# Kernel tuning notes

Measured on AMD Instinct MI355X. Metric: run time of the kernel, lower is better.

## Reference

```python
import jax, jax.numpy as jnp
import numpy as np

B, S, E, H = 4, 2048, 1024, 16
D = E // H  # head dim = 64


def setup_inputs() -> dict:
    key0 = jax.random.key(0)
    ks = jax.random.split(key0, 8)
    key = jax.random.normal(ks[0], (B, S, E), dtype=jnp.float32)
    query = jax.random.normal(ks[1], (B, S, E), dtype=jnp.float32)
    value = jax.random.normal(ks[2], (B, S, E), dtype=jnp.float32)
    # causal mask, broadcastable over heads: [B, 1, S, S]; avoids all-masked rows
    mask = jnp.broadcast_to(jnp.tril(jnp.ones((S, S), dtype=jnp.int32)), (B, 1, S, S))
    sc = 1.0 / np.sqrt(E)
    Wq = jax.random.normal(ks[3], (E, E), dtype=jnp.float32) * sc  # nn.Linear weight [out,in]
    Wk = jax.random.normal(ks[4], (E, E), dtype=jnp.float32) * sc
    Wv = jax.random.normal(ks[5], (E, E), dtype=jnp.float32) * sc
    Wo = jax.random.normal(ks[6], (E, E), dtype=jnp.float32) * sc
    bo = jax.random.normal(ks[7], (E,), dtype=jnp.float32) * 0.01
    return {"key": key, "query": query, "value": value, "mask": mask,
            "Wq": Wq, "Wk": Wk, "Wv": Wv, "Wo": Wo, "bo": bo}


def reference(key, query, value, mask, Wq, Wk, Wv, Wo, bo):
    b, s, _ = key.shape
    sq = query.shape[1]
    # projections (nn.Linear: x @ W^T)
    k = (key @ Wk.T).reshape(b, s, H, D).transpose(0, 2, 1, 3)     # [B,H,S,D]
    q = (query @ Wq.T).reshape(b, sq, H, D).transpose(0, 2, 1, 3)  # [B,H,Sq,D]
    v = (value @ Wv.T).reshape(b, s, H, D).transpose(0, 2, 1, 3)   # [B,H,S,D]
    scores = jnp.einsum('bhqd,bhkd->bhqk', q, k)                   # [B,H,Sq,S]
    # original masks BEFORE scaling (-inf survives the divide)
    scores = jnp.where(mask == 0, -jnp.inf, scores)
    scores = scores / jnp.sqrt(jnp.asarray(D, scores.dtype))
    attn = jax.nn.softmax(scores, axis=-1)
    val = jnp.einsum('bhqk,bhkd->bhqd', attn, v)                   # [B,H,Sq,D]
    val = val.transpose(0, 2, 1, 3).reshape(b, s, H * D)           # [B,S,E]
    return val @ Wo.T + bo
```

## Files before the change

### kernel.cpp

```cpp
#include <hip/hip_runtime.h>
#include <hip/hip_bf16.h>
#include <stdint.h>

#define Bk 4
#define Sk 2048
#define Ek 1024
#define Hk 16
#define Dk 64
#define Mk (Bk*Sk)
#define KVB 64

typedef __hip_bfloat16 bf16;
typedef __attribute__((ext_vector_type(8))) short bf16x8;
typedef __attribute__((ext_vector_type(4))) float f32x4;

__device__ __forceinline__ unsigned short f2bf(float f) {
    __hip_bfloat16 h = __float2bfloat16(f);
    return __builtin_bit_cast(unsigned short, h);
}
__device__ __forceinline__ unsigned pack2bf(float a, float b) {
    return (unsigned)f2bf(a) | ((unsigned)f2bf(b) << 16);
}

__device__ __forceinline__ void gld_lds16(const void* g, void* l) {
    __builtin_amdgcn_global_load_lds(
        (const __attribute__((address_space(1))) unsigned int*)g,
        (__attribute__((address_space(3))) unsigned int*)l, 16, 0, 0);
}

__global__ __launch_bounds__(256)
void conv_qkv(const float* __restrict__ q, const float* __restrict__ k,
              const float* __restrict__ v,
              ushort4* __restrict__ qb, ushort4* __restrict__ kb2,
              ushort4* __restrict__ vb)
{
    const int NQ = (Mk * Ek) / 4;
    int i = blockIdx.x * 256 + threadIdx.x;
    const int tot = 3 * NQ;
    for (; i < tot; i += gridDim.x * 256) {
        const float4* sp; ushort4* dp; int j;
        if (i < NQ)            { sp = (const float4*)q; dp = qb;  j = i; }
        else if (i < 2 * NQ)   { sp = (const float4*)k; dp = kb2; j = i - NQ; }
        else                   { sp = (const float4*)v; dp = vb;  j = i - 2 * NQ; }
        float4 x = sp[j];
        ushort4 o; o.x = f2bf(x.x); o.y = f2bf(x.y); o.z = f2bf(x.z); o.w = f2bf(x.w);
        dp[j] = o;
    }
}

__global__ __launch_bounds__(256)
void conv_w(const float* __restrict__ wq, const float* __restrict__ wk,
            const float* __restrict__ wv, const float* __restrict__ wo,
            ushort4* __restrict__ wqb, ushort4* __restrict__ wkb,
            ushort4* __restrict__ wvb, ushort4* __restrict__ wob)
{
    const int NW = (Ek * Ek) / 4;
    int i = blockIdx.x * 256 + threadIdx.x;
    const int tot = 4 * NW;
    for (; i < tot; i += gridDim.x * 256) {
        int rgn = i / NW, j = i - rgn * NW;
        const float4* sp = rgn == 0 ? (const float4*)wq :
                           rgn == 1 ? (const float4*)wk :
                           rgn == 2 ? (const float4*)wv : (const float4*)wo;
        ushort4* dp = rgn == 0 ? wqb : rgn == 1 ? wkb : rgn == 2 ? wvb : wob;
        float sc = (rgn == 0) ? 0.125f * 1.44269504088896f : 1.0f;
        float4 x = sp[j];
        ushort4 o; o.x = f2bf(x.x * sc); o.y = f2bf(x.y * sc);
        o.z = f2bf(x.z * sc); o.w = f2bf(x.w * sc);
        dp[j] = o;
    }
}

template<int EPI>
__global__ __launch_bounds__(256)
void gemm_bt(const bf16* __restrict__ A, const bf16* __restrict__ Bw,
             void* __restrict__ Cout, const float* __restrict__ bias)
{
    __shared__ bf16 As[128 * 64];
    __shared__ bf16 Bs[128 * 64];
    const int t = threadIdx.x, w = t >> 6, lane = t & 63;
    const int lo = lane & 15, hi = lane >> 4;
    const int wm = w >> 1, wn = w & 1;
    const int n0 = blockIdx.x * 128, m0 = blockIdx.y * 128;

    f32x4 acc[4][4] = {};

    const bf16* Ab = A  + (size_t)m0 * Ek;
    const bf16* Bb = Bw + (size_t)n0 * Ek;

    for (int kt = 0; kt < Ek; kt += 64) {
#pragma unroll
        for (int i = 0; i < 4; ++i) {
            int c = (w * 4 + i) * 64 + lane;
            int r = c >> 3, cb = c & 7, scb = cb ^ (r & 7);
            gld_lds16(Ab + (size_t)r * Ek + kt + scb * 8, &As[(w * 4 + i) * 512]);
            gld_lds16(Bb + (size_t)r * Ek + kt + scb * 8, &Bs[(w * 4 + i) * 512]);
        }
        __syncthreads();
#pragma unroll
        for (int kd = 0; kd < 2; ++kd) {
            bf16x8 av[4], bv[4];
#pragma unroll
            for (int mf = 0; mf < 4; ++mf) {
                int r = wm * 64 + mf * 16 + lo;
                int cb = (kd * 4 + hi) ^ (r & 7);
                av[mf] = *(const bf16x8*)&As[r * 64 + cb * 8];
            }
#pragma unroll
            for (int nf = 0; nf < 4; ++nf) {
                int r = wn * 64 + nf * 16 + lo;
                int cb = (kd * 4 + hi) ^ (r & 7);
                bv[nf] = *(const bf16x8*)&Bs[r * 64 + cb * 8];
            }
#pragma unroll
            for (int mf = 0; mf < 4; ++mf)
#pragma unroll
                for (int nf = 0; nf < 4; ++nf)
                    acc[mf][nf] = __builtin_amdgcn_mfma_f32_16x16x32_bf16(
                        av[mf], bv[nf], acc[mf][nf], 0, 0, 0);
        }
        __syncthreads();
    }
#pragma unroll
    for (int mf = 0; mf < 4; ++mf)
#pragma unroll
        for (int nf = 0; nf < 4; ++nf)
#pragma unroll
            for (int r = 0; r < 4; ++r) {
                int m = m0 + wm * 64 + mf * 16 + hi * 4 + r;
                int n = n0 + wn * 64 + nf * 16 + lo;
                float vv = acc[mf][nf][r];
                if constexpr (EPI == 0) {
                    ((bf16*)Cout)[(size_t)m * Ek + n] = __float2bfloat16(vv);
                } else if constexpr (EPI == 1) {
                    int b = m >> 11, s = m & (Sk - 1);
                    ((bf16*)Cout)[((size_t)(b * 1024 + n)) * Sk + s] = __float2bfloat16(vv);
                } else {
                    ((float*)Cout)[(size_t)m * Ek + n] = vv + bias[n];
                }
            }
}

__global__ __launch_bounds__(64)
void attn_fwd1(const bf16* __restrict__ Qp, const bf16* __restrict__ Kp,
               const bf16* __restrict__ Vt, bf16* __restrict__ AO)
{
    __shared__ bf16 Pl[32 * 64];
    const int lane = threadIdx.x;
    const int lo = lane & 15, hi = lane >> 4;
    const int flat = blockIdx.x;
    const int xcd  = flat & 7;
    const int idx  = flat >> 3;
    const int bh   = xcd * 8 + (idx >> 6);
    const int qt   = 63 - (idx & 63);
    const int b = bh >> 4, h = bh & 15;
    const int q0 = qt * 32;
    const int ntiles = q0 / KVB + 1;

    const bf16* Qg = Qp + (size_t)(b * Sk) * Ek + h * 64;
    const bf16* Kg = Kp + (size_t)(b * Sk) * Ek + h * 64;
    const bf16* Vg = Vt + (size_t)(b * 1024 + h * 64) * Sk;

    bf16x8 qf[2][2];
#pragma unroll
    for (int mf = 0; mf < 2; ++mf)
#pragma unroll
        for (int sl = 0; sl < 2; ++sl)
            qf[mf][sl] = *(const bf16x8*)&Qg[(size_t)(q0 + mf * 16 + lo) * Ek + sl * 32 + hi * 8];

    f32x4 acc[2][4] = {};
    float mrow[2] = { -1e30f, -1e30f };
    float lrow[2] = { 0.f, 0.f };

    for (int kt = 0; kt < ntiles; ++kt) {
        const int kb = kt * KVB;
        bf16x8 kfr[4][2], vfr[4][2];
#pragma unroll
        for (int i = 0; i < 4; ++i) {
            const bf16* kr = &Kg[(size_t)(kb + i * 16 + lo) * Ek + hi * 8];
            kfr[i][0] = *(const bf16x8*)kr;
            kfr[i][1] = *(const bf16x8*)(kr + 32);
            const bf16* vr = &Vg[(size_t)(i * 16 + lo) * Sk + kb + hi * 8];
            vfr[i][0] = *(const bf16x8*)vr;
            vfr[i][1] = *(const bf16x8*)(vr + 32);
        }
        f32x4 sT[4][2] = {};
        __builtin_amdgcn_s_setprio(1);
#pragma unroll
        for (int kf = 0; kf < 4; ++kf)
#pragma unroll
            for (int mf = 0; mf < 2; ++mf) {
                sT[kf][mf] = __builtin_amdgcn_mfma_f32_16x16x32_bf16(kfr[kf][0], qf[mf][0], sT[kf][mf], 0, 0, 0);
                sT[kf][mf] = __builtin_amdgcn_mfma_f32_16x16x32_bf16(kfr[kf][1], qf[mf][1], sT[kf][mf], 0, 0, 0);
            }
        __builtin_amdgcn_s_setprio(0);
        if (kb + KVB > q0) {
#pragma unroll
            for (int kf = 0; kf < 4; ++kf)
#pragma unroll
                for (int mf = 0; mf < 2; ++mf)
#pragma unroll
                    for (int r = 0; r < 4; ++r)
                        if (kb + kf * 16 + hi * 4 + r > q0 + mf * 16 + lo)
                            sT[kf][mf][r] = -1e30f;
        }
        float pmax[2];
#pragma unroll
        for (int mf = 0; mf < 2; ++mf) {
            float v0 = fmaxf(fmaxf(sT[0][mf][0], sT[0][mf][1]), fmaxf(sT[0][mf][2], sT[0][mf][3]));
            float v1 = fmaxf(fmaxf(sT[1][mf][0], sT[1][mf][1]), fmaxf(sT[1][mf][2], sT[1][mf][3]));
            float v2 = fmaxf(fmaxf(sT[2][mf][0], sT[2][mf][1]), fmaxf(sT[2][mf][2], sT[2][mf][3]));
            float v3 = fmaxf(fmaxf(sT[3][mf][0], sT[3][mf][1]), fmaxf(sT[3][mf][2], sT[3][mf][3]));
            float v = fmaxf(fmaxf(v0, v1), fmaxf(v2, v3));
            v = fmaxf(v, __shfl_xor(v, 16));
            v = fmaxf(v, __shfl_xor(v, 32));
            pmax[mf] = v;
        }
        bool need = (pmax[0] > mrow[0] + 8.f) || (pmax[1] > mrow[1] + 8.f);
        if (__any(need)) {
            float sf[2];
#pragma unroll
            for (int mf = 0; mf < 2; ++mf) {
                float mn = fmaxf(mrow[mf], pmax[mf]);
                sf[mf] = exp2f(mrow[mf] - mn);
                mrow[mf] = mn;
                lrow[mf] *= sf[mf];
            }
#pragma unroll
            for (int r = 0; r < 4; ++r) {
                float a0 = __shfl(sf[0], hi * 4 + r);
                float a1 = __shfl(sf[1], hi * 4 + r);
#pragma unroll
                for (int nd = 0; nd < 4; ++nd) { acc[0][nd][r] *= a0; acc[1][nd][r] *= a1; }
            }
        }
        float rs[2] = { 0.f, 0.f };
#pragma unroll
        for (int kf = 0; kf < 4; ++kf)
#pragma unroll
            for (int mf = 0; mf < 2; ++mf)
#pragma unroll
                for (int r = 0; r < 4; ++r) {
                    float p = exp2f(sT[kf][mf][r] - mrow[mf]);
                    sT[kf][mf][r] = p;
                    rs[mf] += p;
                }
#pragma unroll
        for (int mf = 0; mf < 2; ++mf) {
            float v = rs[mf];
            v += __shfl_xor(v, 16);
            v += __shfl_xor(v, 32);
            lrow[mf] += v;
        }
#pragma unroll
        for (int mf = 0; mf < 2; ++mf)
#pragma unroll
            for (int kf = 0; kf < 4; ++kf) {
                int q = mf * 16 + lo;
                int chunk = kf * 2 + (hi >> 1);
                int idx2 = q * 64 + ((chunk ^ (q & 7)) * 8) + 4 * (hi & 1);
                uint2 u;
                u.x = pack2bf(sT[kf][mf][0], sT[kf][mf][1]);
                u.y = pack2bf(sT[kf][mf][2], sT[kf][mf][3]);
                *(uint2*)&Pl[idx2] = u;
            }
        bf16x8 pa[2][2];
#pragma unroll
        for (int mf = 0; mf < 2; ++mf)
#pragma unroll
            for (int ks = 0; ks < 2; ++ks) {
                int q = mf * 16 + lo;
                pa[mf][ks] = *(const bf16x8*)&Pl[q * 64 + (((ks * 4 + hi) ^ (q & 7)) * 8)];
            }
        __builtin_amdgcn_s_setprio(1);
#pragma unroll
        for (int mf = 0; mf < 2; ++mf)
#pragma unroll
            for (int nd = 0; nd < 4; ++nd) {
                acc[mf][nd] = __builtin_amdgcn_mfma_f32_16x16x32_bf16(pa[mf][0], vfr[nd][0], acc[mf][nd], 0, 0, 0);
                acc[mf][nd] = __builtin_amdgcn_mfma_f32_16x16x32_bf16(pa[mf][1], vfr[nd][1], acc[mf][nd], 0, 0, 0);
            }
        __builtin_amdgcn_s_setprio(0);
    }
#pragma unroll
    for (int mf = 0; mf < 2; ++mf)
#pragma unroll
        for (int r = 0; r < 4; ++r) {
            float il = 1.0f / __shfl(lrow[mf], hi * 4 + r);
            int q = q0 + mf * 16 + hi * 4 + r;
#pragma unroll
            for (int nd = 0; nd < 4; ++nd)
                AO[(size_t)(b * Sk + q) * Ek + h * 64 + nd * 16 + lo] =
                    __float2bfloat16(acc[mf][nd][r] * il);
        }
}

extern "C" void kernel_launch(void* const* d_in, const int* in_sizes, int n_in,
                              void* d_out, int out_size, void* d_ws, size_t ws_size,
                              hipStream_t stream)
{
    (void)in_sizes; (void)n_in; (void)out_size; (void)ws_size;
    const float* key   = (const float*)d_in[0];
    const float* query = (const float*)d_in[1];
    const float* value = (const float*)d_in[2];
    const float* Wq = (const float*)d_in[4];
    const float* Wk = (const float*)d_in[5];
    const float* Wv = (const float*)d_in[6];
    const float* Wo = (const float*)d_in[7];
    const float* bo = (const float*)d_in[8];

    char* ws = (char*)d_ws;
    bf16* Vin = (bf16*)ws; ws += (size_t)Mk * Ek * 2;
    bf16* Wqb = (bf16*)ws; ws += (size_t)Ek * Ek * 2;
    bf16* Wkb = (bf16*)ws; ws += (size_t)Ek * Ek * 2;
    bf16* Wvb = (bf16*)ws; ws += (size_t)Ek * Ek * 2;
    bf16* Wob = (bf16*)ws; ws += (size_t)Ek * Ek * 2;
    bf16* Qp  = (bf16*)ws; ws += (size_t)Mk * Ek * 2;
    bf16* Kp  = (bf16*)ws; ws += (size_t)Mk * Ek * 2;
    bf16* Vt  = (bf16*)ws; ws += (size_t)Mk * Ek * 2;
    bf16* AO  = (bf16*)ws; ws += (size_t)Mk * Ek * 2;

    bf16* Qin = (bf16*)d_out;
    bf16* Kin = Qin + (size_t)Mk * Ek;

    conv_qkv<<<4096, 256, 0, stream>>>(query, key, value,
                                       (ushort4*)Qin, (ushort4*)Kin, (ushort4*)Vin);
    conv_w<<<2048, 256, 0, stream>>>(Wq, Wk, Wv, Wo,
                                     (ushort4*)Wqb, (ushort4*)Wkb, (ushort4*)Wvb, (ushort4*)Wob);

    dim3 gg(Ek / 128, Mk / 128);
    gemm_bt<0><<<gg, 256, 0, stream>>>(Qin, Wqb, Qp, nullptr);
    gemm_bt<0><<<gg, 256, 0, stream>>>(Kin, Wkb, Kp, nullptr);
    gemm_bt<1><<<gg, 256, 0, stream>>>(Vin, Wvb, Vt, nullptr);

    attn_fwd1<<<dim3(Sk / 32 * Hk * Bk), 64, 0, stream>>>(Qp, Kp, Vt, AO);

    gemm_bt<2><<<gg, 256, 0, stream>>>(AO, Wob, d_out, bo);
}
```

Baseline: 438.3 us.

## Share K/V tiles across four waves via double-buffered LDS in attention

Replaces the single-wave attention kernel, which loaded K and V straight from global memory into registers, with a 256-thread block of four waves covering 128 queries. The waves share swizzled K/V tiles staged in LDS with global_load_lds and double buffering. This cuts redundant global K/V traffic fourfold and overlaps the next tile's load with compute. The cost is a block-wide barrier every tile and idle waves on causal diagonal tiles. Blocks are also fewer and larger, which may reduce load balance.

```diff
diff --git a/kernel.cpp b/kernel.cpp
--- a/kernel.cpp
+++ b/kernel.cpp
@@ -9,6 +9,7 @@
 #define Dk 64
 #define Mk (Bk*Sk)
 #define KVB 64
+#define QCH 128
 
 typedef __hip_bfloat16 bf16;
 typedef __attribute__((ext_vector_type(8))) short bf16x8;
@@ -141,21 +142,25 @@
             }
 }
 
-__global__ __launch_bounds__(64)
-void attn_fwd1(const bf16* __restrict__ Qp, const bf16* __restrict__ Kp,
-               const bf16* __restrict__ Vt, bf16* __restrict__ AO)
-{
-    __shared__ bf16 Pl[32 * 64];
-    const int lane = threadIdx.x;
+__global__ __launch_bounds__(256)
+void attn_fwd4x(const bf16* __restrict__ Qp, const bf16* __restrict__ Kp,
+                const bf16* __restrict__ Vt, bf16* __restrict__ AO)
+{
+    __shared__ bf16 Kl[2][KVB * 64];
+    __shared__ bf16 Vl[2][64 * KVB];
+    __shared__ bf16 Pl[4][32 * 64];
+    const int t = threadIdx.x, w = t >> 6, lane = t & 63;
     const int lo = lane & 15, hi = lane >> 4;
     const int flat = blockIdx.x;
     const int xcd  = flat & 7;
     const int idx  = flat >> 3;
-    const int bh   = xcd * 8 + (idx >> 6);
-    const int qt   = 63 - (idx & 63);
+    const int bh   = xcd * 8 + (idx >> 4);
+    const int qc   = 15 - (idx & 15);
     const int b = bh >> 4, h = bh & 15;
-    const int q0 = qt * 32;
-    const int ntiles = q0 / KVB + 1;
+    const int qbase = qc * QCH;
+    const int q0 = qbase + w * 32;
+    const int qe = q0 + 32;
+    const int ntiles = (qbase + QCH) / KVB;
 
     const bf16* Qg = Qp + (size_t)(b * Sk) * Ek + h * 64;
     const bf16* Kg = Kp + (size_t)(b * Sk) * Ek + h * 64;
@@ -172,115 +177,138 @@
     float mrow[2] = { -1e30f, -1e30f };
     float lrow[2] = { 0.f, 0.f };
 
+#pragma unroll
+    for (int i = 0; i < 2; ++i) {
+        int c = w * 128 + i * 64 + lane;
+        int r = c >> 3, cb = c & 7, scb = cb ^ (r & 7);
+        gld_lds16(Kg + (size_t)r * Ek + scb * 8, &Kl[0][(w * 128 + i * 64) * 8]);
+        gld_lds16(Vg + (size_t)r * Sk + scb * 8, &Vl[0][(w * 128 + i * 64) * 8]);
+    }
+    __syncthreads();
+
     for (int kt = 0; kt < ntiles; ++kt) {
         const int kb = kt * KVB;
-        bf16x8 kfr[4][2], vfr[4][2];
-#pragma unroll
-        for (int i = 0; i < 4; ++i) {
-            const bf16* kr = &Kg[(size_t)(kb + i * 16 + lo) * Ek + hi * 8];
-            kfr[i][0] = *(const bf16x8*)kr;
-            kfr[i][1] = *(const bf16x8*)(kr + 32);
-            const bf16* vr = &Vg[(size_t)(i * 16 + lo) * Sk + kb + hi * 8];
-            vfr[i][0] = *(const bf16x8*)vr;
-            vfr[i][1] = *(const bf16x8*)(vr + 32);
-        }
-        f32x4 sT[4][2] = {};
-        __builtin_amdgcn_s_setprio(1);
-#pragma unroll
-        for (int kf = 0; kf < 4; ++kf)
+        const int cur = kt & 1;
+        if (kt + 1 < ntiles) {
+            const int kb2 = kb + KVB;
+#pragma unroll
+            for (int i = 0; i < 2; ++i) {
+                int c = w * 128 + i * 64 + lane;
+                int r = c >> 3, cb = c & 7, scb = cb ^ (r & 7);
+                gld_lds16(Kg + (size_t)(kb2 + r) * Ek + scb * 8,
+                          &Kl[cur ^ 1][(w * 128 + i * 64) * 8]);
+                gld_lds16(Vg + (size_t)r * Sk + kb2 + scb * 8,
+                          &Vl[cur ^ 1][(w * 128 + i * 64) * 8]);
+            }
+        }
+        if (kb < qe) {
+            f32x4 sT[4][2] = {};
+            __builtin_amdgcn_s_setprio(1);
+#pragma unroll
+            for (int kf = 0; kf < 4; ++kf) {
+                int rk = kf * 16 + lo;
+                bf16x8 k0 = *(const bf16x8*)&Kl[cur][rk * 64 + ((0 + hi) ^ (rk & 7)) * 8];
+                bf16x8 k1 = *(const bf16x8*)&Kl[cur][rk * 64 + ((4 + hi) ^ (rk & 7)) * 8];
+#pragma unroll
+                for (int mf = 0; mf < 2; ++mf) {
+                    sT[kf][mf] = __builtin_amdgcn_mfma_f32_16x16x32_bf16(k0, qf[mf][0], sT[kf][mf], 0, 0, 0);
+                    sT[kf][mf] = __builtin_amdgcn_mfma_f32_16x16x32_bf16(k1, qf[mf][1], sT[kf][mf], 0, 0, 0);
+                }
+            }
+            __builtin_amdgcn_s_setprio(0);
+            if (kb + KVB > q0) {
+#pragma unroll
+                for (int kf = 0; kf < 4; ++kf)
+#pragma unroll
+                    for (int mf = 0; mf < 2; ++mf)
+#pragma unroll
+                        for (int r = 0; r < 4; ++r)
+                            if (kb + kf * 16 + hi * 4 + r > q0 + mf * 16 + lo)
+                                sT[kf][mf][r] = -1e30f;
+            }
+            float pmax[2];
 #pragma unroll
             for (int mf = 0; mf < 2; ++mf) {
-                sT[kf][mf] = __builtin_amdgcn_mfma_f32_16x16x32_bf16(kfr[kf][0], qf[mf][0], sT[kf][mf], 0, 0, 0);
-                sT[kf][mf] = __builtin_amdgcn_mfma_f32_16x16x32_bf16(kfr[kf][1], qf[mf][1], sT[kf][mf], 0, 0, 0);
-            }
-        __builtin_amdgcn_s_setprio(0);
-        if (kb + KVB > q0) {
+                float v0 = fmaxf(fmaxf(sT[0][mf][0], sT[0][mf][1]), fmaxf(sT[0][mf][2], sT[0][mf][3]));
+                float v1 = fmaxf(fmaxf(sT[1][mf][0], sT[1][mf][1]), fmaxf(sT[1][mf][2], sT[1][mf][3]));
+                float v2 = fmaxf(fmaxf(sT[2][mf][0], sT[2][mf][1]), fmaxf(sT[2][mf][2], sT[2][mf][3]));
+                float v3 = fmaxf(fmaxf(sT[3][mf][0], sT[3][mf][1]), fmaxf(sT[3][mf][2], sT[3][mf][3]));
+                float v = fmaxf(fmaxf(v0, v1), fmaxf(v2, v3));
+                v = fmaxf(v, __shfl_xor(v, 16));
+                v = fmaxf(v, __shfl_xor(v, 32));
+                pmax[mf] = v;
+            }
+            bool need = (pmax[0] > mrow[0] + 8.f) || (pmax[1] > mrow[1] + 8.f);
+            if (__any(need)) {
+                float sf[2];
+#pragma unroll
+                for (int mf = 0; mf < 2; ++mf) {
+                    float mn = fmaxf(mrow[mf], pmax[mf]);
+                    sf[mf] = exp2f(mrow[mf] - mn);
+                    mrow[mf] = mn;
+                    lrow[mf] *= sf[mf];
+                }
+#pragma unroll
+                for (int r = 0; r < 4; ++r) {
+                    float a0 = __shfl(sf[0], hi * 4 + r);
+                    float a1 = __shfl(sf[1], hi * 4 + r);
+#pragma unroll
+                    for (int nd = 0; nd < 4; ++nd) { acc[0][nd][r] *= a0; acc[1][nd][r] *= a1; }
+                }
+            }
+            float rs[2] = { 0.f, 0.f };
 #pragma unroll
             for (int kf = 0; kf < 4; ++kf)
 #pragma unroll
                 for (int mf = 0; mf < 2; ++mf)
 #pragma unroll
-                    for (int r = 0; r < 4; ++r)
-                        if (kb + kf * 16 + hi * 4 + r > q0 + mf * 16 + lo)
-                            sT[kf][mf][r] = -1e30f;
-        }
-        float pmax[2];
-#pragma unroll
-        for (int mf = 0; mf < 2; ++mf) {
-            float v0 = fmaxf(fmaxf(sT[0][mf][0], sT[0][mf][1]), fmaxf(sT[0][mf][2], sT[0][mf][3]));
-            float v1 = fmaxf(fmaxf(sT[1][mf][0], sT[1][mf][1]), fmaxf(sT[1][mf][2], sT[1][mf][3]));
-            float v2 = fmaxf(fmaxf(sT[2][mf][0], sT[2][mf][1]), fmaxf(sT[2][mf][2], sT[2][mf][3]));
-            float v3 = fmaxf(fmaxf(sT[3][mf][0], sT[3][mf][1]), fmaxf(sT[3][mf][2], sT[3][mf][3]));
-            float v = fmaxf(fmaxf(v0, v1), fmaxf(v2, v3));
-            v = fmaxf(v, __shfl_xor(v, 16));
-            v = fmaxf(v, __shfl_xor(v, 32));
-            pmax[mf] = v;
-        }
-        bool need = (pmax[0] > mrow[0] + 8.f) || (pmax[1] > mrow[1] + 8.f);
-        if (__any(need)) {
-            float sf[2];
+                    for (int r = 0; r < 4; ++r) {
+                        float p = exp2f(sT[kf][mf][r] - mrow[mf]);
+                        sT[kf][mf][r] = p;
+                        rs[mf] += p;
+                    }
 #pragma unroll
             for (int mf = 0; mf < 2; ++mf) {
-                float mn = fmaxf(mrow[mf], pmax[mf]);
-                sf[mf] = exp2f(mrow[mf] - mn);
-                mrow[mf] = mn;
-                lrow[mf] *= sf[mf];
-            }
-#pragma unroll
-            for (int r = 0; r < 4; ++r) {
-                float a0 = __shfl(sf[0], hi * 4 + r);
-                float a1 = __shfl(sf[1], hi * 4 + r);
-#pragma unroll
-                for (int nd = 0; nd < 4; ++nd) { acc[0][nd][r] *= a0; acc[1][nd][r] *= a1; }
-            }
-        }
-        float rs[2] = { 0.f, 0.f };
-#pragma unroll
-        for (int kf = 0; kf < 4; ++kf)
+                float v = rs[mf];
+                v += __shfl_xor(v, 16);
+                v += __shfl_xor(v, 32);
+                lrow[mf] += v;
+            }
 #pragma unroll
             for (int mf = 0; mf < 2; ++mf)
 #pragma unroll
-                for (int r = 0; r < 4; ++r) {
-                    float p = exp2f(sT[kf][mf][r] - mrow[mf]);
-                    sT[kf][mf][r] = p;
-                    rs[mf] += p;
-                }
-#pragma unroll
-        for (int mf = 0; mf < 2; ++mf) {
-            float v = rs[mf];
-            v += __shfl_xor(v, 16);
-            v += __shfl_xor(v, 32);
-            lrow[mf] += v;
-        }
-#pragma unroll
-        for (int mf = 0; mf < 2; ++mf)
-#pragma unroll
-            for (int kf = 0; kf < 4; ++kf) {
-                int q = mf * 16 + lo;
-                int chunk = kf * 2 + (hi >> 1);
-                int idx2 = q * 64 + ((chunk ^ (q & 7)) * 8) + 4 * (hi & 1);
-                uint2 u;
-                u.x = pack2bf(sT[kf][mf][0], sT[kf][mf][1]);
-                u.y = pack2bf(sT[kf][mf][2], sT[kf][mf][3]);
-                *(uint2*)&Pl[idx2] = u;
-            }
-        bf16x8 pa[2][2];
-#pragma unroll
-        for (int mf = 0; mf < 2; ++mf)
-#pragma unroll
-            for (int ks = 0; ks < 2; ++ks) {
-                int q = mf * 16 + lo;
-                pa[mf][ks] = *(const bf16x8*)&Pl[q * 64 + (((ks * 4 + hi) ^ (q & 7)) * 8)];
-            }
-        __builtin_amdgcn_s_setprio(1);
-#pragma unroll
-        for (int mf = 0; mf < 2; ++mf)
+                for (int kf = 0; kf < 4; ++kf) {
+                    int q = mf * 16 + lo;
+                    int chunk = kf * 2 + (hi >> 1);
+                    int idx2 = q * 64 + ((chunk ^ (q & 7)) * 8) + 4 * (hi & 1);
+                    uint2 u;
+                    u.x = pack2bf(sT[kf][mf][0], sT[kf][mf][1]);
+                    u.y = pack2bf(sT[kf][mf][2], sT[kf][mf][3]);
+                    *(uint2*)&Pl[w][idx2] = u;
+                }
+            bf16x8 pa[2][2];
+#pragma unroll
+            for (int mf = 0; mf < 2; ++mf)
+#pragma unroll
+                for (int ks = 0; ks < 2; ++ks) {
+                    int q = mf * 16 + lo;
+                    pa[mf][ks] = *(const bf16x8*)&Pl[w][q * 64 + (((ks * 4 + hi) ^ (q & 7)) * 8)];
+                }
+            __builtin_amdgcn_s_setprio(1);
 #pragma unroll
             for (int nd = 0; nd < 4; ++nd) {
-                acc[mf][nd] = __builtin_amdgcn_mfma_f32_16x16x32_bf16(pa[mf][0], vfr[nd][0], acc[mf][nd], 0, 0, 0);
-                acc[mf][nd] = __builtin_amdgcn_mfma_f32_16x16x32_bf16(pa[mf][1], vfr[nd][1], acc[mf][nd], 0, 0, 0);
-            }
-        __builtin_amdgcn_s_setprio(0);
+                int rv = nd * 16 + lo;
+                bf16x8 v0 = *(const bf16x8*)&Vl[cur][rv * 64 + ((0 + hi) ^ (rv & 7)) * 8];
+                bf16x8 v1 = *(const bf16x8*)&Vl[cur][rv * 64 + ((4 + hi) ^ (rv & 7)) * 8];
+#pragma unroll
+                for (int mf = 0; mf < 2; ++mf) {
+                    acc[mf][nd] = __builtin_amdgcn_mfma_f32_16x16x32_bf16(pa[mf][0], v0, acc[mf][nd], 0, 0, 0);
+                    acc[mf][nd] = __builtin_amdgcn_mfma_f32_16x16x32_bf16(pa[mf][1], v1, acc[mf][nd], 0, 0, 0);
+                }
+            }
+            __builtin_amdgcn_s_setprio(0);
+        }
+        __syncthreads();
     }
 #pragma unroll
     for (int mf = 0; mf < 2; ++mf)
@@ -333,7 +361,7 @@
     gemm_bt<0><<<gg, 256, 0, stream>>>(Kin, Wkb, Kp, nullptr);
     gemm_bt<1><<<gg, 256, 0, stream>>>(Vin, Wvb, Vt, nullptr);
 
-    attn_fwd1<<<dim3(Sk / 32 * Hk * Bk), 64, 0, stream>>>(Qp, Kp, Vt, AO);
+    attn_fwd4x<<<dim3((Sk / QCH) * Hk * Bk / 8 * 8), 256, 0, stream>>>(Qp, Kp, Vt, AO);
 
     gemm_bt<2><<<gg, 256, 0, stream>>>(AO, Wob, d_out, bo);
 }
```

Measured after the change: 418.9 us. 4.4% less time.
